# Kernel tuning notes

Measured on AMD Instinct MI355X. Metric: run time of the kernel, lower is better.

The kernel has to match this reference:

```python
import jax, jax.numpy as jnp
import numpy as np

B, N, L, D = 4096, 11, 12, 256
ZDIM = 32
LINE_DIM = 64
PAST_DIM = 6 * D - (2 * D + LINE_DIM)  # 960


def _pos_enc(length, d):
    # PositionalAgentEncoding.build_pos_enc
    pos = jnp.arange(length, dtype=jnp.float32)[:, None]
    div = jnp.exp(jnp.arange(0, d, 2, dtype=jnp.float32) * (-np.log(10000.0) / d))
    pe = jnp.zeros((length, d), dtype=jnp.float32)
    pe = pe.at[:, 0::2].set(jnp.sin(pos * div))
    pe = pe.at[:, 1::2].set(jnp.cos(pos * div))
    return pe


def setup_inputs() -> dict:
    key = jax.random.key(0)
    ks = jax.random.split(key, 16)
    s = 0.02
    return {
        "inputs": jax.random.normal(ks[0], (B * N, L, 4), jnp.float32),
        "past_feature": jax.random.normal(ks[1], (B * N, PAST_DIM), jnp.float32),
        "W_in": jax.random.normal(ks[2], (4, D), jnp.float32) * s,
        "b_in": jnp.zeros((D,), jnp.float32),
        "W_pos": jax.random.normal(ks[3], (2 * D, D), jnp.float32) * s,
        "b_pos": jnp.zeros((D,), jnp.float32),
        "W_fc2": jax.random.normal(ks[4], (L * D, D), jnp.float32) * s,
        "b_fc2": jnp.zeros((D,), jnp.float32),
        "W_fc3": jax.random.normal(ks[5], (D + N, D), jnp.float32) * s,
        "b_fc3": jnp.zeros((D,), jnp.float32),
        "W_msg": jax.random.normal(ks[6], (2 * D, D), jnp.float32) * s,
        "b_msg": jnp.zeros((D,), jnp.float32),
        "W_hyp": jax.random.normal(ks[7], (2 * D, D), jnp.float32) * s,
        "b_hyp": jnp.zeros((D,), jnp.float32),
        "W_line": jax.random.normal(ks[8], (D, LINE_DIM), jnp.float32) * s,
        "W_out": jax.random.normal(ks[9], (6 * D, 128), jnp.float32) * s,
        "b_out": jnp.zeros((128,), jnp.float32),
        "W_qz": jax.random.normal(ks[10], (128, 2 * ZDIM), jnp.float32) * s,
        "b_qz": jnp.zeros((2 * ZDIM,), jnp.float32),
        "batch_size": B,
        "agent_num": N,
    }


def reference(inputs, past_feature, W_in, b_in, W_pos, b_pos, W_fc2, b_fc2,
              W_fc3, b_fc3, W_msg, b_msg, W_hyp, b_hyp, W_line,
              W_out, b_out, W_qz, b_qz, batch_size, agent_num):
    BN, length, _ = inputs.shape
    d = W_in.shape[1]
    bsz, n = batch_size, agent_num
    # input_fc + positional encoding (concat=True, dropout=eval identity)
    tf = inputs @ W_in + b_in                                   # [BN, L, D]
    pe = jnp.broadcast_to(_pos_enc(length, d), (BN, length, d))
    tf = jnp.concatenate([tf, pe], axis=-1) @ W_pos + b_pos     # [BN, L, D]
    # input_fc2 over flattened time, then category concat + input_fc3
    ftraj = tf.reshape(bsz, n, length * d) @ W_fc2 + b_fc2      # [B, N, D]
    cat = jnp.broadcast_to(jnp.eye(n, dtype=ftraj.dtype), (bsz, n, n))
    ftraj = jnp.concatenate([ftraj, cat], axis=-1) @ W_fc3 + b_fc3
    # cosine correlation + per-scene adaptive threshold
    q = ftraj / jnp.linalg.norm(ftraj, axis=2, keepdims=True)
    corr = jnp.einsum('bnd,bmd->bnm', q, q)                     # [B, N, N]
    a = corr.min(axis=(1, 2))
    thr = jnp.where(a < 0.4, 0.4,
                    jnp.where((a > 0.4) & (a < 0.6), a + 0.1, a + 0.03))
    corr = jnp.where(corr < thr[:, None, None], 0.0, corr)
    # ordinary MS_HGNN surrogate: one dense message-passing round
    attn = jax.nn.softmax(jnp.einsum('bnd,bmd->bnm', ftraj, ftraj)
                          / jnp.sqrt(jnp.asarray(d, ftraj.dtype)), axis=-1)
    agg = jnp.einsum('bnm,bmd->bnd', attn, ftraj)
    ftraj_inter = jax.nn.relu(jnp.concatenate([ftraj, agg], -1) @ W_msg + b_msg)
    # hyper/clique surrogate: binarized thresholded corr as incidence, degree-normalized
    A = (corr > 0).astype(ftraj.dtype)
    A = A / jnp.maximum(A.sum(-1, keepdims=True), 1.0)
    hag = jnp.einsum('bnm,bmd->bnd', A, ftraj)
    hyp = jax.nn.relu(jnp.concatenate([ftraj, hag], -1) @ W_hyp + b_hyp)
    feat_bs = hyp @ W_line                                      # [B, N, 64]
    final = jnp.concatenate([ftraj, ftraj_inter, feat_bs], -1).reshape(bsz * n, -1)
    h = jnp.concatenate([past_feature, final], axis=-1)         # [BN, 6D]
    h = jax.nn.relu(h @ W_out + b_out)
    return h @ W_qz + b_qz                                      # [BN, 2*zdim]
```

## Files before the change

kernel.cpp:

```cpp
#include <hip/hip_runtime.h>
#include <hip/hip_bf16.h>

#define BB 4096
#define NNA 11
#define BN (BB*NNA)

#define OFF_WEFF   0
#define OFF_BIASL  1024
#define OFF_WBIG   4096
#define OFF_BIAS2  16384
#define OFF_WALL   16640
#define OFF_BIASN  28928
#define OFF_WG1F   31744
#define OFF_BIASG1 87040
#define OFF_WG2    99712
#define OFF_WQT    198656
#define OFF_P2T    202752
#define OFF_P3T    205824
#define OFF_MIX    296320
#define OFF_INTER  1287552

typedef short bh8 __attribute__((ext_vector_type(8)));
typedef float fx4 __attribute__((ext_vector_type(4)));

__device__ __forceinline__ float b2f(__hip_bfloat16 x) { return __bfloat162float(x); }
__device__ __forceinline__ short f2bs(float v) { __hip_bfloat16 h = __float2bfloat16(v); return *(short*)&h; }


__global__ __launch_bounds__(256) void k_p1(const float* W_in, const float* b_in,
                                            const float* W_pos, const float* b_pos,
                                            float* ws) {
  __shared__ float A[16*512];
  __shared__ float red[4*16*64];
  int t = threadIdx.x, cb = blockIdx.x;
  int ks = t >> 6, c = t & 63, col = cb*64 + c;
  float coef = -logf(10000.f) / 256.f;
  for (int i = t; i < 16*512; i += 256) {
    int row = i >> 9, kk = i & 511;
    float v;
    if (row < 4) v = (kk < 256) ? W_in[row*256 + kk] : 0.f;
    else if (kk < 256) v = b_in[kk];
    else {
      int ii = (kk - 256) >> 1;
      float dv = expf(coef * (float)(2*ii));
      float ang = (float)(row - 4) * dv;
      v = (kk & 1) ? cosf(ang) : sinf(ang);
    }
    A[i] = v;
  }
  __syncthreads();
  float acc[16];
  #pragma unroll
  for (int r = 0; r < 16; ++r) acc[r] = 0.f;
  #pragma unroll 4
  for (int j = 0; j < 128; ++j) {
    int jj = ks*128 + j;
    float b = W_pos[(size_t)jj*256 + col];
    #pragma unroll
    for (int r = 0; r < 16; ++r) acc[r] += A[r*512 + jj] * b;
  }
  #pragma unroll
  for (int r = 0; r < 16; ++r) red[(ks*16 + r)*64 + c] = acc[r];
  __syncthreads();
  for (int i = t; i < 16*64; i += 256) {
    int row = i >> 6, cc = i & 63;
    float s = red[row*64+cc] + red[(16+row)*64+cc] + red[(32+row)*64+cc] + red[(48+row)*64+cc];
    int gcol = cb*64 + cc;
    if (row < 4) ws[OFF_WEFF + row*256 + gcol] = s;
    else         ws[OFF_BIASL + (row-4)*256 + gcol] = s + b_pos[gcol];
  }
}

__global__ __launch_bounds__(256) void k_p2(const float* W_fc2, float* ws) {
  __shared__ float A[5*256];
  __shared__ float red[4*5*64];
  int t = threadIdx.x, cb = blockIdx.x, l = blockIdx.y;
  int ks = t >> 6, c = t & 63, col = cb*64 + c;
  for (int i = t; i < 5*256; i += 256) {
    int row = i >> 8, kk = i & 255;
    A[i] = (row < 4) ? ws[OFF_WEFF + row*256 + kk] : ws[OFF_BIASL + l*256 + kk];
  }
  __syncthreads();
  float acc[5] = {0.f, 0.f, 0.f, 0.f, 0.f};
  #pragma unroll 4
  for (int j = 0; j < 64; ++j) {
    int jj = ks*64 + j;
    float b = W_fc2[(size_t)(l*256 + jj)*256 + col];
    #pragma unroll
    for (int r = 0; r < 5; ++r) acc[r] += A[r*256 + jj] * b;
  }
  #pragma unroll
  for (int r = 0; r < 5; ++r) red[(ks*5 + r)*64 + c] = acc[r];
  __syncthreads();
  for (int i = t; i < 5*64; i += 256) {
    int row = i / 64, cc = i % 64;
    float s = red[row*64+cc] + red[(5+row)*64+cc] + red[(10+row)*64+cc] + red[(15+row)*64+cc];
    int gcol = cb*64 + cc;
    if (row < 4) ws[OFF_WBIG + (l*4 + row)*256 + gcol] = s;
    else         ws[OFF_P2T + l*256 + gcol] = s;
  }
}

__global__ __launch_bounds__(256) void k_p2b(const float* b_fc2, float* ws) {
  int d = threadIdx.x;
  float s = b_fc2[d];
  #pragma unroll
  for (int l = 0; l < 12; ++l) s += ws[OFF_P2T + l*256 + d];
  ws[OFF_BIAS2 + d] = s;
}

__global__ __launch_bounds__(256) void k_p3(const float* W_fc3, float* ws) {
  __shared__ float A[7*256];
  __shared__ float red[4*7*64];
  int t = threadIdx.x, cb = blockIdx.x, rg = blockIdx.y;
  int ks = t >> 6, c = t & 63, col = cb*64 + c;
  for (int i = t; i < 7*256; i += 256) {
    int row = i >> 8, kk = i & 255, gr = rg*7 + row;
    A[i] = (gr < 48) ? ws[OFF_WBIG + gr*256 + kk] : (gr == 48 ? ws[OFF_BIAS2 + kk] : 0.f);
  }
  __syncthreads();
  float acc[7] = {0.f,0.f,0.f,0.f,0.f,0.f,0.f};
  #pragma unroll 4
  for (int j = 0; j < 64; ++j) {
    int jj = ks*64 + j;
    float b = W_fc3[(size_t)jj*256 + col];
    #pragma unroll
    for (int r = 0; r < 7; ++r) acc[r] += A[r*256 + jj] * b;
  }
  #pragma unroll
  for (int r = 0; r < 7; ++r) red[(ks*7 + r)*64 + c] = acc[r];
  __syncthreads();
  for (int i = t; i < 7*64; i += 256) {
    int row = i / 64, cc = i % 64, gr = rg*7 + row;
    float s = red[row*64+cc] + red[(7+row)*64+cc] + red[(14+row)*64+cc] + red[(21+row)*64+cc];
    int gcol = cb*64 + cc;
    if (gr < 48)       ws[OFF_WALL + gr*256 + gcol] = s;
    else if (gr == 48) ws[OFF_P3T + gcol] = s;
  }
}

__global__ __launch_bounds__(256) void k_p3b(const float* W_fc3, const float* b_fc3, float* ws) {
  int d = threadIdx.x, n = blockIdx.x;
  ws[OFF_BIASN + n*256 + d] = ws[OFF_P3T + d] + b_fc3[d] + W_fc3[(size_t)(256+n)*256 + d];
}

__device__ __forceinline__ float wg1_elem(int j, int col, const float* W_msg,
                                          const float* W_hyp, const float* W_out) {
  if (col < 256)       return W_msg[j*256 + col];
  else if (col < 512)  return W_msg[(256+j)*256 + (col-256)];
  else if (col < 768)  return W_hyp[j*256 + (col-512)];
  else if (col < 1024) return W_hyp[(256+j)*256 + (col-768)];
  else                 return W_out[(960+j)*128 + (col-1024)];
}

__global__ __launch_bounds__(256) void k_p4(const float* W_msg, const float* b_msg,
                                            const float* W_hyp, const float* b_hyp,
                                            const float* W_out, float* ws) {
  __shared__ float A[8*256];
  __shared__ float red[4*8*64];
  int t = threadIdx.x, cb = blockIdx.x, rg = blockIdx.y;
  int ks = t >> 6, c = t & 63, col = cb*64 + c;
  for (int i = t; i < 8*256; i += 256) {
    int row = i >> 8, kk = i & 255, gr = rg*8 + row;
    A[i] = (gr < 48) ? ws[OFF_WALL + gr*256 + kk]
         : (gr < 59 ? ws[OFF_BIASN + (gr-48)*256 + kk] : 0.f);
  }
  __syncthreads();
  float acc[8];
  #pragma unroll
  for (int r = 0; r < 8; ++r) acc[r] = 0.f;
  #pragma unroll 4
  for (int j = 0; j < 64; ++j) {
    int jj = ks*64 + j;
    float b = wg1_elem(jj, col, W_msg, W_hyp, W_out);
    #pragma unroll
    for (int r = 0; r < 8; ++r) acc[r] += A[r*256 + jj] * b;
  }
  #pragma unroll
  for (int r = 0; r < 8; ++r) red[(ks*8 + r)*64 + c] = acc[r];
  __syncthreads();
  for (int i = t; i < 8*64; i += 256) {
    int row = i >> 6, cc = i & 63, gr = rg*8 + row;
    float s = red[row*64+cc] + red[(8+row)*64+cc] + red[(16+row)*64+cc] + red[(24+row)*64+cc];
    int gcol = cb*64 + cc;
    if (gr < 48) {
      ws[OFF_WG1F + gr*1152 + gcol] = s;
    } else if (gr < 59) {
      if (gcol < 256) s += b_msg[gcol];
      else if (gcol >= 512 && gcol < 768) s += b_hyp[gcol-512];
      ws[OFF_BIASG1 + (gr-48)*1152 + gcol] = s;
    }
  }
}

__global__ __launch_bounds__(128) void k_p5(const float* W_line, const float* W_out,
                                            float* ws) {
  int c = threadIdx.x, r = blockIdx.x;
  float v;
  if (r < 960)       v = W_out[r*128 + c];
  else if (r < 1216) v = W_out[(r+256)*128 + c];
  else if (r < 1472) {
    int dd = r - 1216;
    float s = 0.f;
    for (int j = 0; j < 64; ++j)
      s += W_line[dd*64 + j] * W_out[(1472+j)*128 + c];
    v = s;
  } else if (r < 1520) {
    v = ws[OFF_WG1F + (r-1472)*1152 + 1024 + c];
  } else v = 0.f;
  short* WTs = (short*)(ws + OFF_WG2);
  WTs[(size_t)c*1536 + r] = f2bs(v);
}

__global__ __launch_bounds__(256) void k_p6(const float* W_qz, float* ws) {
  int i = blockIdx.x*256 + threadIdx.x;
  int n = i >> 7, k = i & 127;
  short* WQs = (short*)(ws + OFF_WQT);
  WQs[n*128 + k] = f2bs(W_qz[k*64 + n]);
}

__global__ __launch_bounds__(256) void k_front(const float* inputs, float* ws) {
  __shared__ float XT[48*44];
  __shared__ float F[44*260];
  __shared__ float C[4*121];
  int t = threadIdx.x;
  int R0 = blockIdx.x * 44;
  for (int i = t; i < 44*48; i += 256) {
    int r = i / 48, k = i - r*48;
    XT[k*44 + r] = inputs[(size_t)(R0+r)*48 + k];
  }
  __syncthreads();
  {
    int d = t;
    float acc[44];
    #pragma unroll
    for (int r = 0; r < 44; ++r) acc[r] = ws[OFF_BIASN + (r % 11)*256 + d];
    for (int k = 0; k < 48; ++k) {
      float w = ws[OFF_WALL + k*256 + d];
      #pragma unroll
      for (int j = 0; j < 11; ++j) {
        float4 xv = *(const float4*)&XT[k*44 + 4*j];
        acc[4*j+0] += xv.x*w; acc[4*j+1] += xv.y*w;
        acc[4*j+2] += xv.z*w; acc[4*j+3] += xv.w*w;
      }
    }
    #pragma unroll
    for (int r = 0; r < 44; ++r) F[r*260 + d] = acc[r];
  }
  __syncthreads();
  int w = t >> 6, lane = t & 63;
  {
    const float4* F4 = (const float4*)F;
    for (int p = lane; p < 66; p += 64) {
      int n = 0, pp = p;
      while (pp >= 11 - n) { pp -= 11 - n; ++n; }
      int m = n + pp;
      int ra = (w*11 + n) * 65, rb2 = (w*11 + m) * 65;
      float s = 0.f;
      #pragma unroll 4
      for (int j = 0; j < 64; ++j) {
        float4 a = F4[ra + j], b = F4[rb2 + j];
        s += a.x*b.x + a.y*b.y + a.z*b.z + a.w*b.w;
      }
      C[w*121 + n*11 + m] = s;
      C[w*121 + m*11 + n] = s;
    }
  }
  __syncthreads();
  {
    float* Cw = C + w*121;
    float rn[11];
    #pragma unroll
    for (int n = 0; n < 11; ++n) rn[n] = 1.f / sqrtf(Cw[n*11+n]);
    float a = 1e30f;
    for (int n = 0; n < 11; ++n)
      for (int m = 0; m < 11; ++m)
        a = fminf(a, Cw[n*11+m] * rn[n] * rn[m]);
    float thr = (a < 0.4f) ? 0.4f : (((a > 0.4f) && (a < 0.6f)) ? a + 0.1f : a + 0.03f);
    int scene = blockIdx.x*4 + w;
    float* mixb = ws + OFF_MIX + (size_t)scene*242;
    if (lane < 11) {
      int n = lane;
      float mx = -1e30f;
      #pragma unroll
      for (int m = 0; m < 11; ++m) mx = fmaxf(mx, Cw[n*11+m]);
      mx *= (1.f/16.f);
      float e[11], ssum = 0.f;
      #pragma unroll
      for (int m = 0; m < 11; ++m) { e[m] = expf(Cw[n*11+m]*(1.f/16.f) - mx); ssum += e[m]; }
      float inv = 1.f / ssum;
      #pragma unroll
      for (int m = 0; m < 11; ++m) mixb[n*11+m] = e[m]*inv;
      float keep[11], cnt = 0.f;
      #pragma unroll
      for (int m = 0; m < 11; ++m) {
        float q = Cw[n*11+m] * rn[n] * rn[m];
        keep[m] = (q >= thr) ? 1.f : 0.f; cnt += keep[m];
      }
      float sc = 1.f / fmaxf(cnt, 1.f);
      #pragma unroll
      for (int m = 0; m < 11; ++m) mixb[121 + n*11 + m] = keep[m]*sc;
    }
  }
}

__global__ __launch_bounds__(256) void k_mix(const float* inputs, float* ws,
                                             __hip_bfloat16* outI, __hip_bfloat16* outH) {
  __shared__ float XT[48*24];
  __shared__ float MW[2*121];
  int t = threadIdx.x;
  int s0 = blockIdx.x * 2;
  int R0 = s0 * 11;
  int gy = blockIdx.y;
  __hip_bfloat16* dst = gy ? outH : outI;
  for (int i = t; i < 22*48; i += 256) {
    int r = i / 48, k = i - r*48;
    XT[k*24 + r] = inputs[(size_t)(R0+r)*48 + k];
  }
  for (int i = t; i < 96; i += 256) { int k = i >> 1, r = 22 + (i & 1); XT[k*24+r] = 0.f; }
  for (int i = t; i < 242; i += 256) {
    int s = i / 121, j = i - s*121;
    MW[i] = ws[OFF_MIX + (size_t)(s0+s)*242 + gy*121 + j];
  }
  __syncthreads();
  int gc = gy*512 + t;
  float accT[24], accB[24];
  #pragma unroll
  for (int r = 0; r < 24; ++r) {
    if (r < 22) {
      accT[r] = ws[OFF_BIASG1 + (r % 11)*1152 + gc];
      accB[r] = ws[OFF_BIASG1 + (r % 11)*1152 + gc + 256];
    } else { accT[r] = 0.f; accB[r] = 0.f; }
  }
  for (int k = 0; k < 48; ++k) {
    float wt = ws[OFF_WG1F + k*1152 + gc];
    float wb = ws[OFF_WG1F + k*1152 + gc + 256];
    #pragma unroll
    for (int j = 0; j < 6; ++j) {
      float4 xv = *(const float4*)&XT[k*24 + 4*j];
      accT[4*j+0] += xv.x*wt; accT[4*j+1] += xv.y*wt; accT[4*j+2] += xv.z*wt; accT[4*j+3] += xv.w*wt;
      accB[4*j+0] += xv.x*wb; accB[4*j+1] += xv.y*wb; accB[4*j+2] += xv.z*wb; accB[4*j+3] += xv.w*wb;
    }
  }
  #pragma unroll
  for (int s = 0; s < 2; ++s)
    #pragma unroll
    for (int n = 0; n < 11; ++n) {
      float v = accT[s*11+n];
      #pragma unroll
      for (int m = 0; m < 11; ++m)
        v += MW[s*121 + n*11 + m] * accB[s*11+m];
      v = fmaxf(v, 0.f);
      dst[(size_t)(R0 + s*11 + n)*256 + t] = __float2bfloat16(v);
    }
}

#define A_OFF 0
#define BT_OFF 4608
#define HS_OFF 0
#define WQ_OFF 8704
__global__ __launch_bounds__(256) void k_g2(const float* past, const float* inputs,
                                            const float* b_out, const float* b_qz,
                                            const __hip_bfloat16* interI, const __hip_bfloat16* hypI,
                                            float* ws, float* out) {
  __shared__ short LDS[18432];
  int t = threadIdx.x;
  int R0 = blockIdx.x * 64;
  int w = t >> 6, lane = t & 63, quad = lane >> 4, l16 = lane & 15;
  const short* WTs = (const short*)(ws + OFF_WG2);
  const short* WQs = (const short*)(ws + OFF_WQT);
  const short* intS = (const short*)interI;
  const short* hypS = (const short*)hypI;

  fx4 acc[4][2];
  #pragma unroll
  for (int mt = 0; mt < 4; ++mt)
    #pragma unroll
    for (int reg = 0; reg < 4; ++reg) {
      int nidx = (R0 + mt*16 + quad*4 + reg) % 11;
      #pragma unroll
      for (int nt = 0; nt < 2; ++nt) {
        int col = w*32 + nt*16 + l16;
        acc[mt][nt][reg] = b_out[col] + ws[OFF_BIASG1 + nidx*1152 + 1024 + col];
      }
    }

  int ar = t >> 2, akq = (t & 3) * 16;
  int bn = t >> 1, bkh = (t & 1) * 32;
  for (int ch = 0; ch < 24; ++ch) {
    __syncthreads();
    {
      short tmp[16];
      if (ch < 15) {
        const float4* sp = (const float4*)(past + (size_t)(R0+ar)*960 + ch*64 + akq);
        #pragma unroll
        for (int q = 0; q < 4; ++q) {
          float4 v = sp[q];
          tmp[4*q+0]=f2bs(v.x); tmp[4*q+1]=f2bs(v.y); tmp[4*q+2]=f2bs(v.z); tmp[4*q+3]=f2bs(v.w);
        }
        *(bh8*)&LDS[A_OFF + ar*72 + akq]     = *(bh8*)&tmp[0];
        *(bh8*)&LDS[A_OFF + ar*72 + akq + 8] = *(bh8*)&tmp[8];
      } else if (ch < 23) {
        const short* s = ((ch < 19) ? intS : hypS) + (size_t)(R0+ar)*256 + ((ch < 19) ? (ch-15) : (ch-19))*64 + akq;
        *(bh8*)&LDS[A_OFF + ar*72 + akq]     = *(const bh8*)&s[0];
        *(bh8*)&LDS[A_OFF + ar*72 + akq + 8] = *(const bh8*)&s[8];
      } else {
        if (akq < 48) {
          const float4* sp = (const float4*)(inputs + (size_t)(R0+ar)*48 + akq);
          #pragma unroll
          for (int q = 0; q < 4; ++q) {
            float4 v = sp[q];
            tmp[4*q+0]=f2bs(v.x); tmp[4*q+1]=f2bs(v.y); tmp[4*q+2]=f2bs(v.z); tmp[4*q+3]=f2bs(v.w);
          }
        } else {
          #pragma unroll
          for (int q = 0; q < 16; ++q) tmp[q] = 0;
        }
        *(bh8*)&LDS[A_OFF + ar*72 + akq]     = *(bh8*)&tmp[0];
        *(bh8*)&LDS[A_OFF + ar*72 + akq + 8] = *(bh8*)&tmp[8];
      }
    }
    {
      const short* s = WTs + (size_t)bn*1536 + ch*64 + bkh;
      #pragma unroll
      for (int q = 0; q < 4; ++q)
        *(bh8*)&LDS[BT_OFF + bn*72 + bkh + q*8] = *(const bh8*)&s[q*8];
    }
    __syncthreads();
    #pragma unroll
    for (int ks = 0; ks < 2; ++ks) {
      int kk = ks*32 + quad*8;
      bh8 a[4], b[2];
      #pragma unroll
      for (int mt = 0; mt < 4; ++mt) a[mt] = *(const bh8*)&LDS[A_OFF + (mt*16 + l16)*72 + kk];
      #pragma unroll
      for (int nt = 0; nt < 2; ++nt) b[nt] = *(const bh8*)&LDS[BT_OFF + (w*32 + nt*16 + l16)*72 + kk];
      #pragma unroll
      for (int mt = 0; mt < 4; ++mt)
        #pragma unroll
        for (int nt = 0; nt < 2; ++nt)
          acc[mt][nt] = __builtin_amdgcn_mfma_f32_16x16x32_bf16(a[mt], b[nt], acc[mt][nt], 0, 0, 0);
    }
  }
  __syncthreads();
  #pragma unroll
  for (int mt = 0; mt < 4; ++mt)
    #pragma unroll
    for (int nt = 0; nt < 2; ++nt)
      #pragma unroll
      for (int reg = 0; reg < 4; ++reg)
        LDS[HS_OFF + (mt*16 + quad*4 + reg)*136 + w*32 + nt*16 + l16] = f2bs(fmaxf(acc[mt][nt][reg], 0.f));
  {
    int n = t >> 2, kh = (t & 3) * 32;
    const short* s = WQs + n*128 + kh;
    #pragma unroll
    for (int q = 0; q < 4; ++q)
      *(bh8*)&LDS[WQ_OFF + n*136 + kh + q*8] = *(const bh8*)&s[q*8];
  }
  __syncthreads();
  fx4 acc2[4];
  {
    float bq = b_qz[w*16 + l16];
    #pragma unroll
    for (int mt = 0; mt < 4; ++mt) { acc2[mt][0]=bq; acc2[mt][1]=bq; acc2[mt][2]=bq; acc2[mt][3]=bq; }
  }
  #pragma unroll
  for (int ks = 0; ks < 4; ++ks) {
    int kk = ks*32 + quad*8;
    bh8 bb = *(const bh8*)&LDS[WQ_OFF + (w*16 + l16)*136 + kk];
    #pragma unroll
    for (int mt = 0; mt < 4; ++mt) {
      bh8 aa = *(const bh8*)&LDS[HS_OFF + (mt*16 + l16)*136 + kk];
      acc2[mt] = __builtin_amdgcn_mfma_f32_16x16x32_bf16(aa, bb, acc2[mt], 0, 0, 0);
    }
  }
  #pragma unroll
  for (int mt = 0; mt < 4; ++mt)
    #pragma unroll
    for (int reg = 0; reg < 4; ++reg)
      out[(size_t)(R0 + mt*16 + quad*4 + reg)*64 + w*16 + l16] = acc2[mt][reg];
}

extern "C" void kernel_launch(void* const* d_in, const int* in_sizes, int n_in,
                              void* d_out, int out_size, void* d_ws, size_t ws_size,
                              hipStream_t stream) {
  const float* inputs = (const float*)d_in[0];
  const float* past   = (const float*)d_in[1];
  const float* W_in   = (const float*)d_in[2];
  const float* b_in   = (const float*)d_in[3];
  const float* W_pos  = (const float*)d_in[4];
  const float* b_pos  = (const float*)d_in[5];
  const float* W_fc2  = (const float*)d_in[6];
  const float* b_fc2  = (const float*)d_in[7];
  const float* W_fc3  = (const float*)d_in[8];
  const float* b_fc3  = (const float*)d_in[9];
  const float* W_msg  = (const float*)d_in[10];
  const float* b_msg  = (const float*)d_in[11];
  const float* W_hyp  = (const float*)d_in[12];
  const float* b_hyp  = (const float*)d_in[13];
  const float* W_line = (const float*)d_in[14];
  const float* W_out  = (const float*)d_in[15];
  const float* b_out  = (const float*)d_in[16];
  const float* W_qz   = (const float*)d_in[17];
  const float* b_qz   = (const float*)d_in[18];
  float* ws = (float*)d_ws;
  __hip_bfloat16* interI = (__hip_bfloat16*)(ws + OFF_INTER);
  __hip_bfloat16* hypI   = interI + (size_t)BN*256;
  float* outp   = (float*)d_out;

  hipLaunchKernelGGL(k_p1,  dim3(4),      dim3(256), 0, stream, W_in, b_in, W_pos, b_pos, ws);
  hipLaunchKernelGGL(k_p2,  dim3(4, 12),  dim3(256), 0, stream, W_fc2, ws);
  hipLaunchKernelGGL(k_p2b, dim3(1),      dim3(256), 0, stream, b_fc2, ws);
  hipLaunchKernelGGL(k_p3,  dim3(4, 7),   dim3(256), 0, stream, W_fc3, ws);
  hipLaunchKernelGGL(k_p3b, dim3(11),     dim3(256), 0, stream, W_fc3, b_fc3, ws);
  hipLaunchKernelGGL(k_p4,  dim3(18, 8),  dim3(256), 0, stream, W_msg, b_msg, W_hyp, b_hyp, W_out, ws);
  hipLaunchKernelGGL(k_p5,  dim3(1536),   dim3(128), 0, stream, W_line, W_out, ws);
  hipLaunchKernelGGL(k_p6,  dim3(32),     dim3(256), 0, stream, W_qz, ws);
  hipLaunchKernelGGL(k_front, dim3(1024), dim3(256), 0, stream, inputs, ws);
  hipLaunchKernelGGL(k_mix, dim3(2048, 2), dim3(256), 0, stream, inputs, ws, interI, hypI);
  hipLaunchKernelGGL(k_g2,  dim3(704),    dim3(256), 0, stream, past, inputs, b_out, b_qz,
                     interI, hypI, ws, outp);
}
```

Measured before the change: 515.8 us.

## Move k_mix projection to bf16 MFMA and double k_g2 row tile

k_mix's scalar FP32 projection of inputs into message/hyper features is replaced by a bf16 MFMA GEMM. It uses a transposed bf16 weight copy built in k_p4/k_p6, and the per-agent bias is folded in as one-hot columns of the A matrix. Intermediate results are staged in LDS as bf16 before the 11x11 mixing, and each block handles 4 scenes instead of 2. k_g2 now processes 128 rows per block instead of 64, halving the grid and reusing each weight tile across more rows at the cost of more registers and LDS. Rounding the inputs and intermediates to bf16 adds precision loss.

```diff
diff --git a/kernel.cpp b/kernel.cpp
--- a/kernel.cpp
+++ b/kernel.cpp
@@ -17,6 +17,7 @@
 #define OFF_WQT    198656
 #define OFF_P2T    202752
 #define OFF_P3T    205824
+#define OFF_WG1FT  206080
 #define OFF_MIX    296320
 #define OFF_INTER  1287552
 
@@ -25,6 +26,7 @@
 
 __device__ __forceinline__ float b2f(__hip_bfloat16 x) { return __bfloat162float(x); }
 __device__ __forceinline__ short f2bs(float v) { __hip_bfloat16 h = __float2bfloat16(v); return *(short*)&h; }
+__device__ __forceinline__ float s2f(short s) { return __bfloat162float(*(__hip_bfloat16*)&s); }
 
 
 __global__ __launch_bounds__(256) void k_p1(const float* W_in, const float* b_in,
@@ -179,16 +181,19 @@
   #pragma unroll
   for (int r = 0; r < 8; ++r) red[(ks*8 + r)*64 + c] = acc[r];
   __syncthreads();
+  short* WG1FTs = (short*)(ws + OFF_WG1FT);
   for (int i = t; i < 8*64; i += 256) {
     int row = i >> 6, cc = i & 63, gr = rg*8 + row;
     float s = red[row*64+cc] + red[(8+row)*64+cc] + red[(16+row)*64+cc] + red[(24+row)*64+cc];
     int gcol = cb*64 + cc;
     if (gr < 48) {
       ws[OFF_WG1F + gr*1152 + gcol] = s;
+      if (gcol < 1024) WG1FTs[(size_t)gcol*64 + gr] = f2bs(s);
     } else if (gr < 59) {
       if (gcol < 256) s += b_msg[gcol];
       else if (gcol >= 512 && gcol < 768) s += b_hyp[gcol-512];
       ws[OFF_BIASG1 + (gr-48)*1152 + gcol] = s;
+      if (gcol < 1024) WG1FTs[(size_t)gcol*64 + gr] = f2bs(s);
     }
   }
 }
@@ -214,9 +219,16 @@
 
 __global__ __launch_bounds__(256) void k_p6(const float* W_qz, float* ws) {
   int i = blockIdx.x*256 + threadIdx.x;
-  int n = i >> 7, k = i & 127;
-  short* WQs = (short*)(ws + OFF_WQT);
-  WQs[n*128 + k] = f2bs(W_qz[k*64 + n]);
+  if (i < 8192) {
+    int n = i >> 7, k = i & 127;
+    short* WQs = (short*)(ws + OFF_WQT);
+    WQs[n*128 + k] = f2bs(W_qz[k*64 + n]);
+  } else {
+    int j = i - 8192;
+    int col = j / 5, k = 59 + (j % 5);
+    short* WG1FTs = (short*)(ws + OFF_WG1FT);
+    WG1FTs[(size_t)col*64 + k] = 0;
+  }
 }
 
 __global__ __launch_bounds__(256) void k_front(const float* inputs, float* ws) {
@@ -306,75 +318,104 @@
 
 __global__ __launch_bounds__(256) void k_mix(const float* inputs, float* ws,
                                              __hip_bfloat16* outI, __hip_bfloat16* outH) {
-  __shared__ float XT[48*24];
-  __shared__ float MW[2*121];
+  __shared__ short A[48*72];
+  __shared__ short P[48*520];
   int t = threadIdx.x;
-  int s0 = blockIdx.x * 2;
-  int R0 = s0 * 11;
   int gy = blockIdx.y;
+  int S0 = blockIdx.x * 4;
+  int R0 = S0 * 11;
+  int w = t >> 6, lane = t & 63, quad = lane >> 4, l16 = lane & 15;
+  const short* WG1FTs = (const short*)(ws + OFF_WG1FT);
+
+  for (int i = t; i < 384; i += 256) {
+    int r = i >> 3, k8 = (i & 7) * 8;
+    short tmp[8];
+    if (r < 44 && k8 < 48) {
+      const float4* sp = (const float4*)(inputs + (size_t)(R0 + r)*48 + k8);
+      float4 v0 = sp[0], v1 = sp[1];
+      tmp[0]=f2bs(v0.x); tmp[1]=f2bs(v0.y); tmp[2]=f2bs(v0.z); tmp[3]=f2bs(v0.w);
+      tmp[4]=f2bs(v1.x); tmp[5]=f2bs(v1.y); tmp[6]=f2bs(v1.z); tmp[7]=f2bs(v1.w);
+    } else if (r < 44) {
+      int a = r % 11;
+      #pragma unroll
+      for (int j = 0; j < 8; ++j) tmp[j] = (k8 + j == 48 + a) ? (short)0x3F80 : (short)0;
+    } else {
+      #pragma unroll
+      for (int j = 0; j < 8; ++j) tmp[j] = 0;
+    }
+    *(bh8*)&A[r*72 + k8] = *(bh8*)tmp;
+  }
+  __syncthreads();
+
+  fx4 acc[3][8];
+  #pragma unroll
+  for (int mt = 0; mt < 3; ++mt)
+    #pragma unroll
+    for (int nt = 0; nt < 8; ++nt) acc[mt][nt] = (fx4){0.f, 0.f, 0.f, 0.f};
+  #pragma unroll
+  for (int ks = 0; ks < 2; ++ks) {
+    int kk = ks*32 + quad*8;
+    bh8 a[3], b[8];
+    #pragma unroll
+    for (int mt = 0; mt < 3; ++mt) a[mt] = *(const bh8*)&A[(mt*16 + l16)*72 + kk];
+    #pragma unroll
+    for (int nt = 0; nt < 8; ++nt) {
+      int col = gy*512 + w*128 + nt*16 + l16;
+      b[nt] = *(const bh8*)&WG1FTs[(size_t)col*64 + kk];
+    }
+    #pragma unroll
+    for (int mt = 0; mt < 3; ++mt)
+      #pragma unroll
+      for (int nt = 0; nt < 8; ++nt)
+        acc[mt][nt] = __builtin_amdgcn_mfma_f32_16x16x32_bf16(a[mt], b[nt], acc[mt][nt], 0, 0, 0);
+  }
+  #pragma unroll
+  for (int mt = 0; mt < 3; ++mt)
+    #pragma unroll
+    for (int nt = 0; nt < 8; ++nt)
+      #pragma unroll
+      for (int reg = 0; reg < 4; ++reg)
+        P[(mt*16 + quad*4 + reg)*520 + w*128 + nt*16 + l16] = f2bs(acc[mt][nt][reg]);
+  __syncthreads();
+
   __hip_bfloat16* dst = gy ? outH : outI;
-  for (int i = t; i < 22*48; i += 256) {
-    int r = i / 48, k = i - r*48;
-    XT[k*24 + r] = inputs[(size_t)(R0+r)*48 + k];
-  }
-  for (int i = t; i < 96; i += 256) { int k = i >> 1, r = 22 + (i & 1); XT[k*24+r] = 0.f; }
-  for (int i = t; i < 242; i += 256) {
-    int s = i / 121, j = i - s*121;
-    MW[i] = ws[OFF_MIX + (size_t)(s0+s)*242 + gy*121 + j];
-  }
-  __syncthreads();
-  int gc = gy*512 + t;
-  float accT[24], accB[24];
-  #pragma unroll
-  for (int r = 0; r < 24; ++r) {
-    if (r < 22) {
-      accT[r] = ws[OFF_BIASG1 + (r % 11)*1152 + gc];
-      accB[r] = ws[OFF_BIASG1 + (r % 11)*1152 + gc + 256];
-    } else { accT[r] = 0.f; accB[r] = 0.f; }
-  }
-  for (int k = 0; k < 48; ++k) {
-    float wt = ws[OFF_WG1F + k*1152 + gc];
-    float wb = ws[OFF_WG1F + k*1152 + gc + 256];
-    #pragma unroll
-    for (int j = 0; j < 6; ++j) {
-      float4 xv = *(const float4*)&XT[k*24 + 4*j];
-      accT[4*j+0] += xv.x*wt; accT[4*j+1] += xv.y*wt; accT[4*j+2] += xv.z*wt; accT[4*j+3] += xv.w*wt;
-      accB[4*j+0] += xv.x*wb; accB[4*j+1] += xv.y*wb; accB[4*j+2] += xv.z*wb; accB[4*j+3] += xv.w*wb;
-    }
-  }
-  #pragma unroll
-  for (int s = 0; s < 2; ++s)
+  int c = t;
+  #pragma unroll
+  for (int s = 0; s < 4; ++s) {
+    float pb[11];
+    #pragma unroll
+    for (int m = 0; m < 11; ++m) pb[m] = s2f(P[(s*11 + m)*520 + 256 + c]);
+    const float* mw = ws + OFF_MIX + (size_t)(S0 + s)*242 + gy*121;
     #pragma unroll
     for (int n = 0; n < 11; ++n) {
-      float v = accT[s*11+n];
-      #pragma unroll
-      for (int m = 0; m < 11; ++m)
-        v += MW[s*121 + n*11 + m] * accB[s*11+m];
-      v = fmaxf(v, 0.f);
-      dst[(size_t)(R0 + s*11 + n)*256 + t] = __float2bfloat16(v);
-    }
+      float v = s2f(P[(s*11 + n)*520 + c]);
+      #pragma unroll
+      for (int m = 0; m < 11; ++m) v += mw[n*11 + m] * pb[m];
+      dst[(size_t)(R0 + s*11 + n)*256 + c] = __float2bfloat16(fmaxf(v, 0.f));
+    }
+  }
 }
 
 #define A_OFF 0
-#define BT_OFF 4608
+#define BT_OFF 9216
 #define HS_OFF 0
-#define WQ_OFF 8704
+#define WQ_OFF 17408
 __global__ __launch_bounds__(256) void k_g2(const float* past, const float* inputs,
                                             const float* b_out, const float* b_qz,
                                             const __hip_bfloat16* interI, const __hip_bfloat16* hypI,
                                             float* ws, float* out) {
-  __shared__ short LDS[18432];
+  __shared__ short LDS[26112];
   int t = threadIdx.x;
-  int R0 = blockIdx.x * 64;
+  int R0 = blockIdx.x * 128;
   int w = t >> 6, lane = t & 63, quad = lane >> 4, l16 = lane & 15;
   const short* WTs = (const short*)(ws + OFF_WG2);
   const short* WQs = (const short*)(ws + OFF_WQT);
   const short* intS = (const short*)interI;
   const short* hypS = (const short*)hypI;
 
-  fx4 acc[4][2];
-  #pragma unroll
-  for (int mt = 0; mt < 4; ++mt)
+  fx4 acc[8][2];
+  #pragma unroll
+  for (int mt = 0; mt < 8; ++mt)
     #pragma unroll
     for (int reg = 0; reg < 4; ++reg) {
       int nidx = (R0 + mt*16 + quad*4 + reg) % 11;
@@ -385,39 +426,42 @@
       }
     }
 
-  int ar = t >> 2, akq = (t & 3) * 16;
+  int ar = t >> 1, akh = (t & 1) * 32;
   int bn = t >> 1, bkh = (t & 1) * 32;
   for (int ch = 0; ch < 24; ++ch) {
     __syncthreads();
     {
-      short tmp[16];
+      short tmp[32];
       if (ch < 15) {
-        const float4* sp = (const float4*)(past + (size_t)(R0+ar)*960 + ch*64 + akq);
+        const float4* sp = (const float4*)(past + (size_t)(R0+ar)*960 + ch*64 + akh);
         #pragma unroll
-        for (int q = 0; q < 4; ++q) {
+        for (int q = 0; q < 8; ++q) {
           float4 v = sp[q];
           tmp[4*q+0]=f2bs(v.x); tmp[4*q+1]=f2bs(v.y); tmp[4*q+2]=f2bs(v.z); tmp[4*q+3]=f2bs(v.w);
         }
-        *(bh8*)&LDS[A_OFF + ar*72 + akq]     = *(bh8*)&tmp[0];
-        *(bh8*)&LDS[A_OFF + ar*72 + akq + 8] = *(bh8*)&tmp[8];
+        #pragma unroll
+        for (int q = 0; q < 4; ++q)
+          *(bh8*)&LDS[A_OFF + ar*72 + akh + q*8] = *(bh8*)&tmp[q*8];
       } else if (ch < 23) {
-        const short* s = ((ch < 19) ? intS : hypS) + (size_t)(R0+ar)*256 + ((ch < 19) ? (ch-15) : (ch-19))*64 + akq;
-        *(bh8*)&LDS[A_OFF + ar*72 + akq]     = *(const bh8*)&s[0];
-        *(bh8*)&LDS[A_OFF + ar*72 + akq + 8] = *(const bh8*)&s[8];
+        const short* s = ((ch < 19) ? intS : hypS) + (size_t)(R0+ar)*256 + ((ch < 19) ? (ch-15) : (ch-19))*64 + akh;
+        #pragma unroll
+        for (int q = 0; q < 4; ++q)
+          *(bh8*)&LDS[A_OFF + ar*72 + akh + q*8] = *(const bh8*)&s[q*8];
       } else {
-        if (akq < 48) {
-          const float4* sp = (const float4*)(inputs + (size_t)(R0+ar)*48 + akq);
-          #pragma unroll
-          for (int q = 0; q < 4; ++q) {
-            float4 v = sp[q];
-            tmp[4*q+0]=f2bs(v.x); tmp[4*q+1]=f2bs(v.y); tmp[4*q+2]=f2bs(v.z); tmp[4*q+3]=f2bs(v.w);
+        #pragma unroll
+        for (int q = 0; q < 4; ++q) {
+          int k8 = akh + q*8;
+          if (k8 < 48) {
+            const float4* sp = (const float4*)(inputs + (size_t)(R0+ar)*48 + k8);
+            float4 v0 = sp[0], v1 = sp[1];
+            tmp[0]=f2bs(v0.x); tmp[1]=f2bs(v0.y); tmp[2]=f2bs(v0.z); tmp[3]=f2bs(v0.w);
+            tmp[4]=f2bs(v1.x); tmp[5]=f2bs(v1.y); tmp[6]=f2bs(v1.z); tmp[7]=f2bs(v1.w);
+          } else {
+            #pragma unroll
+            for (int j = 0; j < 8; ++j) tmp[j] = 0;
           }
-        } else {
-          #pragma unroll
-          for (int q = 0; q < 16; ++q) tmp[q] = 0;
+          *(bh8*)&LDS[A_OFF + ar*72 + k8] = *(bh8*)&tmp[0];
         }
-        *(bh8*)&LDS[A_OFF + ar*72 + akq]     = *(bh8*)&tmp[0];
-        *(bh8*)&LDS[A_OFF + ar*72 + akq + 8] = *(bh8*)&tmp[8];
       }
     }
     {
@@ -430,13 +474,13 @@
     #pragma unroll
     for (int ks = 0; ks < 2; ++ks) {
       int kk = ks*32 + quad*8;
-      bh8 a[4], b[2];
-      #pragma unroll
-      for (int mt = 0; mt < 4; ++mt) a[mt] = *(const bh8*)&LDS[A_OFF + (mt*16 + l16)*72 + kk];
+      bh8 a[8], b[2];
+      #pragma unroll
+      for (int mt = 0; mt < 8; ++mt) a[mt] = *(const bh8*)&LDS[A_OFF + (mt*16 + l16)*72 + kk];
       #pragma unroll
       for (int nt = 0; nt < 2; ++nt) b[nt] = *(const bh8*)&LDS[BT_OFF + (w*32 + nt*16 + l16)*72 + kk];
       #pragma unroll
-      for (int mt = 0; mt < 4; ++mt)
+      for (int mt = 0; mt < 8; ++mt)
         #pragma unroll
         for (int nt = 0; nt < 2; ++nt)
           acc[mt][nt] = __builtin_amdgcn_mfma_f32_16x16x32_bf16(a[mt], b[nt], acc[mt][nt], 0, 0, 0);
@@ -444,7 +488,7 @@
   }
   __syncthreads();
   #pragma unroll
-  for (int mt = 0; mt < 4; ++mt)
+  for (int mt = 0; mt < 8; ++mt)
     #pragma unroll
     for (int nt = 0; nt < 2; ++nt)
       #pragma unroll
@@ -458,24 +502,24 @@
       *(bh8*)&LDS[WQ_OFF + n*136 + kh + q*8] = *(const bh8*)&s[q*8];
   }
   __syncthreads();
-  fx4 acc2[4];
+  fx4 acc2[8];
   {
     float bq = b_qz[w*16 + l16];
     #pragma unroll
-    for (int mt = 0; mt < 4; ++mt) { acc2[mt][0]=bq; acc2[mt][1]=bq; acc2[mt][2]=bq; acc2[mt][3]=bq; }
+    for (int mt = 0; mt < 8; ++mt) { acc2[mt][0]=bq; acc2[mt][1]=bq; acc2[mt][2]=bq; acc2[mt][3]=bq; }
   }
   #pragma unroll
   for (int ks = 0; ks < 4; ++ks) {
     int kk = ks*32 + quad*8;
     bh8 bb = *(const bh8*)&LDS[WQ_OFF + (w*16 + l16)*136 + kk];
     #pragma unroll
-    for (int mt = 0; mt < 4; ++mt) {
+    for (int mt = 0; mt < 8; ++mt) {
       bh8 aa = *(const bh8*)&LDS[HS_OFF + (mt*16 + l16)*136 + kk];
       acc2[mt] = __builtin_amdgcn_mfma_f32_16x16x32_bf16(aa, bb, acc2[mt], 0, 0, 0);
     }
   }
   #pragma unroll
-  for (int mt = 0; mt < 4; ++mt)
+  for (int mt = 0; mt < 8; ++mt)
     #pragma unroll
     for (int reg = 0; reg < 4; ++reg)
       out[(size_t)(R0 + mt*16 + quad*4 + reg)*64 + w*16 + l16] = acc2[mt][reg];
@@ -515,9 +559,9 @@
   hipLaunchKernelGGL(k_p3b, dim3(11),     dim3(256), 0, stream, W_fc3, b_fc3, ws);
   hipLaunchKernelGGL(k_p4,  dim3(18, 8),  dim3(256), 0, stream, W_msg, b_msg, W_hyp, b_hyp, W_out, ws);
   hipLaunchKernelGGL(k_p5,  dim3(1536),   dim3(128), 0, stream, W_line, W_out, ws);
-  hipLaunchKernelGGL(k_p6,  dim3(32),     dim3(256), 0, stream, W_qz, ws);
+  hipLaunchKernelGGL(k_p6,  dim3(52),     dim3(256), 0, stream, W_qz, ws);
   hipLaunchKernelGGL(k_front, dim3(1024), dim3(256), 0, stream, inputs, ws);
-  hipLaunchKernelGGL(k_mix, dim3(2048, 2), dim3(256), 0, stream, inputs, ws, interI, hypI);
-  hipLaunchKernelGGL(k_g2,  dim3(704),    dim3(256), 0, stream, past, inputs, b_out, b_qz,
+  hipLaunchKernelGGL(k_mix, dim3(1024, 2), dim3(256), 0, stream, inputs, ws, interI, hypI);
+  hipLaunchKernelGGL(k_g2,  dim3(352),    dim3(256), 0, stream, past, inputs, b_out, b_qz,
                      interI, hypI, ws, outp);
 }
```

Result: no change. 522.2 us (+1.3%).
